# Optimization experiments

Measured on AMD Instinct MI355X. Metric: run time of the kernel, lower is better.

## Reference

```python
import jax, jax.numpy as jnp
import numpy as np

N_NODES = 8192
N_EDGES = 65536
MUL = 16          # multiplicity of 0e and 1o irreps
NB = 16           # num_radial_basis
HID = 16          # num_radial_dimension
MAX_RADIUS = 5.0
SQRT3 = float(np.sqrt(3.0))


def soft_unit_step(x):
    # e3nn.math.soft_unit_step: exp(-1/x) for x>0 else 0 (grad-safe where)
    safe = jnp.where(x > 0, x, 1.0)
    return jnp.where(x > 0, jnp.exp(-1.0 / safe), 0.0)


def setup_inputs() -> dict:
    key = jax.random.key(0)
    ks = jax.random.split(key, 12)
    f_in = jax.random.normal(ks[0], (N_NODES, 4 * MUL), jnp.float32)
    edge_vec = jax.random.normal(ks[1], (N_EDGES, 3), jnp.float32) * 1.5
    edge_src = jax.random.randint(ks[2], (N_EDGES,), 0, N_NODES)
    edge_dst = jax.random.randint(ks[3], (N_EDGES,), 0, N_NODES)
    Wq0 = jax.random.normal(ks[4], (MUL, MUL), jnp.float32)
    Wq1 = jax.random.normal(ks[5], (MUL, MUL), jnp.float32)
    Wk1 = jax.random.normal(ks[6], (NB, HID), jnp.float32)
    Wk2 = jax.random.normal(ks[7], (HID, 4 * MUL * MUL), jnp.float32)
    Wv1 = jax.random.normal(ks[8], (NB, HID), jnp.float32)
    Wv2 = jax.random.normal(ks[9], (HID, 4 * MUL * MUL), jnp.float32)
    Wd0 = jax.random.normal(ks[10], (MUL, MUL), jnp.float32)
    Wd1 = jax.random.normal(ks[11], (MUL, MUL), jnp.float32)
    return dict(f_in=f_in, edge_vec=edge_vec, edge_src=edge_src, edge_dst=edge_dst,
                Wq0=Wq0, Wq1=Wq1, Wk1=Wk1, Wk2=Wk2, Wv1=Wv1, Wv2=Wv2, Wd0=Wd0, Wd1=Wd1)


def _forward(f_in, edge_vec, edge_src, edge_dst,
             Wq0, Wq1, Wk1, Wk2, Wv1, Wv2, Wd0, Wd1):
    f0 = f_in[:, :MUL]                         # [N, MUL]    0e scalars
    f1 = f_in[:, MUL:].reshape(-1, MUL, 3)     # [N, MUL, 3] 1o vectors

    r = jnp.linalg.norm(edge_vec, axis=1)      # [E]
    u = edge_vec / r[:, None]
    sh1 = SQRT3 * u                            # Y_1, component norm (|Y1|^2 = 3); Y_0 = 1

    # soft_one_hot_linspace, basis='smooth_finite', cutoff=True, * sqrt(NB)
    values = jnp.linspace(0.0, MAX_RADIUS, NB + 2)
    step = values[1] - values[0]
    diff = (r[:, None] - values[1:-1]) / step
    C = 1.14136 * float(np.exp(2.0))
    rb = (C * soft_unit_step(diff + 1.0) * soft_unit_step(1.0 - diff)) * np.sqrt(NB)

    edge_cut = soft_unit_step(10.0 * (1.0 - r / MAX_RADIUS))  # [E]

    def mlp(x, W1, W2):  # e3nn FullyConnectedNet with fan-in normalization
        h = jax.nn.silu(x @ (W1 / np.sqrt(NB)))
        return h @ (W2 / np.sqrt(HID))

    wk = mlp(rb, Wk1, Wk2).reshape(-1, 4, MUL, MUL)  # per-edge TP weights
    wv = mlp(rb, Wv1, Wv2).reshape(-1, 4, MUL, MUL)

    # h_q: per-irrep linear
    q0 = f0 @ Wq0 / np.sqrt(MUL)
    q1 = jnp.einsum('nic,io->noc', f1, Wq1) / np.sqrt(MUL)

    x0 = f0[edge_src]   # [E, MUL]
    x1 = f1[edge_src]   # [E, MUL, 3]

    def fctp(w):
        # FullyConnectedTensorProduct (16x0e+16x1o) x (0e+1o) -> (16x0e+16x1o)
        # 4 paths: 0x0->0, 1x1->0 (dot/sqrt3), 0x1->1, 1x0->1
        a = 1.0 / np.sqrt(2 * MUL)
        o0 = jnp.einsum('eij,ei->ej', w[:, 0], x0) \
           + jnp.einsum('eij,eic,ec->ej', w[:, 1], x1, sh1) / SQRT3
        o1 = jnp.einsum('eij,ei,ec->ejc', w[:, 2], x0, sh1) \
           + jnp.einsum('eij,eic->ejc', w[:, 3], x1)
        return o0 * a, o1 * a

    k0, k1 = fctp(wk)
    v0, v1 = fctp(wv)

    # dot_product: FCTP(query, key) -> 0e
    ad = 1.0 / np.sqrt(2.0 * MUL * MUL)
    dot = ad * (jnp.einsum('ij,ei,ej->e', Wd0, q0[edge_dst], k0)
                + jnp.einsum('ij,eic,ejc->e', Wd1, q1[edge_dst], k1) / SQRT3)

    exp = edge_cut * jnp.exp(dot)                                   # [E]
    z = jax.ops.segment_sum(exp, edge_dst, num_segments=N_NODES)    # [N]
    z = jnp.where(z == 0.0, 1.0, z)
    alpha = exp / z[edge_dst]
    # alpha.relu().sqrt() with grad-safe sqrt at 0
    s = jnp.where(alpha > 0, jnp.sqrt(jnp.where(alpha > 0, alpha, 1.0)), 0.0)

    f_out0 = jax.ops.segment_sum(s[:, None] * v0, edge_dst, num_segments=N_NODES)
    f_out1 = jax.ops.segment_sum(s[:, None, None] * v1, edge_dst, num_segments=N_NODES)
    return jnp.concatenate([f_out0, f_out1.reshape(-1, MUL * 3)], axis=-1)  # [N, 64]


def reference(f_in, edge_vec, edge_src, edge_dst,
              Wq0, Wq1, Wk1, Wk2, Wv1, Wv2, Wd0, Wd1):
    return _forward(f_in, edge_vec, edge_src, edge_dst,
                    Wq0, Wq1, Wk1, Wk2, Wv1, Wv2, Wd0, Wd1)
```

## Files before the change

kernel.cpp:

```cpp
#include <hip/hip_runtime.h>
#include <hip/hip_bf16.h>

#define N_NODES 8192
#define N_EDGES 65536
#define BUCKET  48

#define CNT_OFF  0
#define WF_OFF   8192
#define QDI_OFF  24576
#define EXP_OFF  548864
#define VH_OFF   942080

typedef _Float16 half8 __attribute__((ext_vector_type(8)));
typedef float f32x4 __attribute__((ext_vector_type(4)));

__device__ __forceinline__ float sus_f(float x) { return x > 0.f ? __expf(-1.f / x) : 0.f; }
__device__ __forceinline__ float silu_f(float x) { return x / (1.f + __expf(-x)); }

__device__ __forceinline__ half8 vmul(half8 v, _Float16 s) {
    half8 r;
#pragma unroll
    for (int d = 0; d < 8; ++d) r[d] = v[d] * s;
    return r;
}

__global__ __launch_bounds__(256) void k_prep(
    const float* __restrict__ f_in,
    const float* __restrict__ Wq0, const float* __restrict__ Wq1,
    const float* __restrict__ Wd0, const float* __restrict__ Wd1,
    const float* __restrict__ Wk2, const float* __restrict__ Wv2,
    half8* __restrict__ wfrag, float* __restrict__ qdi) {
    __shared__ float f0s[16][16];
    __shared__ float f1s[16][48];
    __shared__ float t0s[16][16];
    __shared__ float t1s[16][48];
    const int blk = blockIdx.x;
    const int tid = threadIdx.x;

    if (blk < 16) {
        int g = blk * 256 + tid;
        int lane = g & 63, t = (g >> 6) & 7, b = (g >> 9) & 3, kv = g >> 11;
        const float* src = kv ? Wv2 : Wk2;
        int n = lane & 15, quad = lane >> 4;
        const float SC = 0.044194173824159216f;
        half8 out;
#pragma unroll
        for (int d = 0; d < 8; ++d) {
            int k = t * 32 + quad * 8 + d;
            int i = k & 15, h = k >> 4;
            out[d] = (_Float16)(src[h * 1024 + b * 256 + i * 16 + n] * SC);
        }
        wfrag[g] = out;
        return;
    }
    const int j = tid & 15, ln = tid >> 4;
    const int n = (blk - 16) * 16 + ln;
    f0s[ln][j]         = f_in[n * 64 + j];
    f1s[ln][j * 3 + 0] = f_in[n * 64 + 16 + j * 3 + 0];
    f1s[ln][j * 3 + 1] = f_in[n * 64 + 16 + j * 3 + 1];
    f1s[ln][j * 3 + 2] = f_in[n * 64 + 16 + j * 3 + 2];
    __syncthreads();
    float t0 = 0.f, ta = 0.f, tb = 0.f, tc = 0.f;
#pragma unroll
    for (int p = 0; p < 16; ++p) {
        float wq0 = Wq0[p * 16 + j];
        float wq1 = Wq1[p * 16 + j];
        t0 += f0s[ln][p] * wq0;
        ta += f1s[ln][p * 3 + 0] * wq1;
        tb += f1s[ln][p * 3 + 1] * wq1;
        tc += f1s[ln][p * 3 + 2] * wq1;
    }
    t0s[ln][j] = t0;
    t1s[ln][j * 3 + 0] = ta; t1s[ln][j * 3 + 1] = tb; t1s[ln][j * 3 + 2] = tc;
    __syncthreads();
    float q0a = 0.f, qa = 0.f, qb = 0.f, qc = 0.f;
#pragma unroll
    for (int i = 0; i < 16; ++i) {
        float wd0 = Wd0[i * 16 + j];
        float wd1 = Wd1[i * 16 + j];
        q0a += t0s[ln][i] * wd0;
        qa  += t1s[ln][i * 3 + 0] * wd1;
        qb  += t1s[ln][i * 3 + 1] * wd1;
        qc  += t1s[ln][i * 3 + 2] * wd1;
    }
    const float S0 = 0.011048543456f;
    const float S1 = 0.0063788674817f;
    float4 q = {q0a * S0, qa * S1, qb * S1, qc * S1};
    ((float4*)qdi)[n * 16 + j] = q;
}

__global__ __launch_bounds__(256) void k_edge(
    const float* __restrict__ f_in, const float* __restrict__ evec,
    const int* __restrict__ esrc, const int* __restrict__ edst,
    const float* __restrict__ Wk1, const float* __restrict__ Wv1,
    const half8* __restrict__ wfrag,
    const float* __restrict__ qdi,
    int* __restrict__ cursor, float* __restrict__ expbuf, _Float16* __restrict__ vh) {
    __shared__ __align__(16) char s_arena[19456];
    _Float16 (*s_x0h)[24] = (_Float16(*)[24])(s_arena);
    _Float16 (*s_xsh)[24] = (_Float16(*)[24])(s_arena + 3072);
    _Float16 (*s_x1h0)[24] = (_Float16(*)[24])(s_arena + 6144);
    _Float16 (*s_x1h1)[24] = (_Float16(*)[24])(s_arena + 9216);
    _Float16 (*s_x1h2)[24] = (_Float16(*)[24])(s_arena + 12288);
    _Float16 (*s_hkh)[16] = (_Float16(*)[16])(s_arena + 15360);
    _Float16 (*s_hvh)[16] = (_Float16(*)[16])(s_arena + 17408);
    _Float16 (*s_vt)[72]  = (_Float16(*)[72])(s_arena);
    __shared__ float s_rb[64][16];
    __shared__ float s_sh[64][4];
    __shared__ int   s_slot[64];

    const int tid = threadIdx.x;
    const int e0 = blockIdx.x * 64;

    {
        const int el = tid >> 2, q = tid & 3;
        const int e = e0 + el;
        float v0 = evec[e * 3 + 0];
        float v1 = evec[e * 3 + 1];
        float v2 = evec[e * 3 + 2];
        float r = sqrtf(v0 * v0 + v1 * v1 + v2 * v2);
        float rs = r * 3.4f;
#pragma unroll
        for (int bb = 0; bb < 4; ++bb) {
            int b = q * 4 + bb;
            s_rb[el][b] = 33.734292f * sus_f(rs - (float)b) * sus_f((float)(b + 2) - rs);
        }
        if (q == 0) {
            float inv = r > 0.f ? 1.f / r : 0.f;
            const float SQ3 = 1.7320508075688772f;
            s_sh[el][0] = SQ3 * v0 * inv;
            s_sh[el][1] = SQ3 * v1 * inv;
            s_sh[el][2] = SQ3 * v2 * inv;
            s_sh[el][3] = sus_f(10.f - 2.f * r);
        }
    }
    __syncthreads();

    {
        const int j = tid & 15, slot = tid >> 4;
        _Float16* xp = (_Float16*)(s_arena + 6144);
#pragma unroll
        for (int s = 0; s < 4; ++s) {
            const int el = slot * 4 + s;
            const int e = e0 + el;
            float aK = 0.f, aV = 0.f;
#pragma unroll
            for (int b = 0; b < 16; ++b) {
                float rbv = s_rb[el][b];
                aK += rbv * Wk1[b * 16 + j];
                aV += rbv * Wv1[b * 16 + j];
            }
            s_hkh[el][(j & 1) * 8 + (j >> 1)] = (_Float16)silu_f(aK * 0.25f);
            s_hvh[el][(j & 1) * 8 + (j >> 1)] = (_Float16)silu_f(aV * 0.25f);
            const int src = esrc[e];
            float4 v4 = ((const float4*)f_in)[src * 16 + j];
            if (j < 4) {
#pragma unroll
                for (int d = 0; d < 4; ++d)
                    s_x0h[el][j * 4 + d] = (_Float16)((&v4.x)[d]);
            } else {
                const int cc = j * 4 - 16;
#pragma unroll
                for (int d = 0; d < 4; ++d) {
                    int c = cc + d;
                    int i = c / 3, comp = c - 3 * i;
                    xp[comp * 1536 + el * 24 + i] = (_Float16)((&v4.x)[d]);
                }
            }
        }
    }
    __syncthreads();

    {
        const int j = tid & 15, slot = tid >> 4;
#pragma unroll
        for (int s = 0; s < 4; ++s) {
            const int el = slot * 4 + s;
            float xa = (float)s_x1h0[el][j];
            float xb = (float)s_x1h1[el][j];
            float xc = (float)s_x1h2[el][j];
            s_xsh[el][j] = (_Float16)((xa * s_sh[el][0] + xb * s_sh[el][1] + xc * s_sh[el][2])
                                      * 0.57735026919f);
        }
    }
    __syncthreads();

    const int lane = tid & 63;
    const int wv = tid >> 6;
    const int m = lane & 15, quad = lane >> 4;
    const int eb = wv * 16;
    const int eloc = eb + m;
    const int ihalf = quad >> 1;
    const int hh = (quad & 1) * 8;

    half8 X0 = *(const half8*)&s_x0h[eloc][hh];
    half8 XS = *(const half8*)&s_xsh[eloc][hh];
    half8 Xa = *(const half8*)&s_x1h0[eloc][hh];
    half8 Xb = *(const half8*)&s_x1h1[eloc][hh];
    half8 Xc = *(const half8*)&s_x1h2[eloc][hh];
    half8 HK = *(const half8*)&s_hkh[eloc][ihalf * 8];
    half8 HV = *(const half8*)&s_hvh[eloc][ihalf * 8];
    __syncthreads();

    {
        f32x4 o0 = {0.f, 0.f, 0.f, 0.f}, a1 = o0, ax = o0, ay = o0, az = o0;
#pragma unroll
        for (int t = 0; t < 8; ++t) {
            _Float16 hs = HK[t];
            half8 B0 = wfrag[(0 * 8 + t) * 64 + lane];
            half8 B1 = wfrag[(1 * 8 + t) * 64 + lane];
            half8 B2 = wfrag[(2 * 8 + t) * 64 + lane];
            half8 B3 = wfrag[(3 * 8 + t) * 64 + lane];
            half8 A0 = vmul(X0, hs);
            half8 As = vmul(XS, hs);
            half8 Aa = vmul(Xa, hs);
            half8 Ab = vmul(Xb, hs);
            half8 Ac = vmul(Xc, hs);
            o0 = __builtin_amdgcn_mfma_f32_16x16x32_f16(A0, B0, o0, 0, 0, 0);
            o0 = __builtin_amdgcn_mfma_f32_16x16x32_f16(As, B1, o0, 0, 0, 0);
            a1 = __builtin_amdgcn_mfma_f32_16x16x32_f16(A0, B2, a1, 0, 0, 0);
            ax = __builtin_amdgcn_mfma_f32_16x16x32_f16(Aa, B3, ax, 0, 0, 0);
            ay = __builtin_amdgcn_mfma_f32_16x16x32_f16(Ab, B3, ay, 0, 0, 0);
            az = __builtin_amdgcn_mfma_f32_16x16x32_f16(Ac, B3, az, 0, 0, 0);
        }
        const int j = m;
#pragma unroll
        for (int r = 0; r < 4; ++r) {
            const int el = eb + quad * 4 + r;
            const int e = e0 + el;
            const int dst = edst[e];
            float sh0 = s_sh[el][0], sh1 = s_sh[el][1], sh2 = s_sh[el][2];
            float k1x = a1[r] * sh0 + ax[r];
            float k1y = a1[r] * sh1 + ay[r];
            float k1z = a1[r] * sh2 + az[r];
            float4 q = ((const float4*)qdi)[dst * 16 + j];
            float dp = q.x * o0[r] + q.y * k1x + q.z * k1y + q.w * k1z;
            dp += __shfl_xor(dp, 1);
            dp += __shfl_xor(dp, 2);
            dp += __shfl_xor(dp, 4);
            dp += __shfl_xor(dp, 8);
            if (j == 0) {
                float ev = s_sh[el][3] * __expf(dp);
                int local = atomicAdd(cursor + dst, 1);
                int slot = dst * BUCKET + local;
                s_slot[el] = slot;
                expbuf[slot] = ev;
            }
        }
    }

    {
        f32x4 o0 = {0.f, 0.f, 0.f, 0.f}, a1 = o0, ax = o0, ay = o0, az = o0;
        const half8* wfv = wfrag + 32 * 64;
#pragma unroll
        for (int t = 0; t < 8; ++t) {
            _Float16 hs = HV[t];
            half8 B0 = wfv[(0 * 8 + t) * 64 + lane];
            half8 B1 = wfv[(1 * 8 + t) * 64 + lane];
            half8 B2 = wfv[(2 * 8 + t) * 64 + lane];
            half8 B3 = wfv[(3 * 8 + t) * 64 + lane];
            half8 A0 = vmul(X0, hs);
            half8 As = vmul(XS, hs);
            half8 Aa = vmul(Xa, hs);
            half8 Ab = vmul(Xb, hs);
            half8 Ac = vmul(Xc, hs);
            o0 = __builtin_amdgcn_mfma_f32_16x16x32_f16(A0, B0, o0, 0, 0, 0);
            o0 = __builtin_amdgcn_mfma_f32_16x16x32_f16(As, B1, o0, 0, 0, 0);
            a1 = __builtin_amdgcn_mfma_f32_16x16x32_f16(A0, B2, a1, 0, 0, 0);
            ax = __builtin_amdgcn_mfma_f32_16x16x32_f16(Aa, B3, ax, 0, 0, 0);
            ay = __builtin_amdgcn_mfma_f32_16x16x32_f16(Ab, B3, ay, 0, 0, 0);
            az = __builtin_amdgcn_mfma_f32_16x16x32_f16(Ac, B3, az, 0, 0, 0);
        }
        const int j = m;
#pragma unroll
        for (int r = 0; r < 4; ++r) {
            const int el = eb + quad * 4 + r;
            float sh0 = s_sh[el][0], sh1 = s_sh[el][1], sh2 = s_sh[el][2];
            s_vt[el][j] = (_Float16)o0[r];
            s_vt[el][16 + j * 3 + 0] = (_Float16)(a1[r] * sh0 + ax[r]);
            s_vt[el][16 + j * 3 + 1] = (_Float16)(a1[r] * sh1 + ay[r]);
            s_vt[el][16 + j * 3 + 2] = (_Float16)(a1[r] * sh2 + az[r]);
        }
    }
    __syncthreads();

#pragma unroll
    for (int pass = 0; pass < 2; ++pass) {
        int row = pass * 32 + (tid >> 3);
        int part = tid & 7;
        half8 val = *(const half8*)&s_vt[row][part * 8];
        int slot = s_slot[row];
        *(half8*)(vh + (size_t)slot * 64 + part * 8) = val;
    }
}

__global__ __launch_bounds__(256) void k_out(
    const int* __restrict__ cnt,
    const float* __restrict__ expbuf, const _Float16* __restrict__ vh,
    float* __restrict__ fout) {
    const int col = threadIdx.x & 63;
    const int n = blockIdx.x * 4 + (threadIdx.x >> 6);
    const int deg = cnt[n];
    const int s0 = n * BUCKET;
    float zs = 0.f;
    float acc = 0.f;
    for (int i = 0; i < deg; ++i) {
        float ev = expbuf[s0 + i];
        zs += ev;
        acc += sqrtf(ev) * (float)vh[(size_t)(s0 + i) * 64 + col];
    }
    float scale = zs > 0.f ? rsqrtf(zs) : 0.f;
    fout[n * 64 + col] = acc * scale;
}

extern "C" void kernel_launch(void* const* d_in, const int* in_sizes, int n_in,
                              void* d_out, int out_size, void* d_ws, size_t ws_size,
                              hipStream_t stream) {
    const float* f_in = (const float*)d_in[0];
    const float* evec = (const float*)d_in[1];
    const int* esrc = (const int*)d_in[2];
    const int* edst = (const int*)d_in[3];
    const float* Wq0 = (const float*)d_in[4];
    const float* Wq1 = (const float*)d_in[5];
    const float* Wk1 = (const float*)d_in[6];
    const float* Wk2 = (const float*)d_in[7];
    const float* Wv1 = (const float*)d_in[8];
    const float* Wv2 = (const float*)d_in[9];
    const float* Wd0 = (const float*)d_in[10];
    const float* Wd1 = (const float*)d_in[11];

    float* ws     = (float*)d_ws;
    int*   cnt    = (int*)(ws + CNT_OFF);
    half8* wfrag  = (half8*)(ws + WF_OFF);
    float* qdi    = ws + QDI_OFF;
    float* expb   = ws + EXP_OFF;
    _Float16* vh  = (_Float16*)(ws + VH_OFF);
    float* fout   = (float*)d_out;

    hipMemsetAsync(cnt, 0, (size_t)8192 * sizeof(int), stream);

    k_prep<<<528, 256, 0, stream>>>(f_in, Wq0, Wq1, Wd0, Wd1, Wk2, Wv2, wfrag, qdi);
    k_edge<<<N_EDGES / 64, 256, 0, stream>>>(f_in, evec, esrc, edst, Wk1, Wv1,
                                             wfrag, qdi, cnt, expb, vh);
    k_out<<<N_NODES / 4, 256, 0, stream>>>(cnt, expb, vh, fout);
}
```

Before: 110.5 us.

## Fold counter memset into prep kernel, compute XS in registers, prefetch queries

Removes the separate hipMemsetAsync by having one prep block zero the bucket counters, saving a launch. In the edge kernel the projected vector term XS is now built in registers from the per-edge spherical harmonics, which drops a shared-memory array, a pass and a barrier. Destination indices and query vectors are loaded before the MFMA loop so their global latency overlaps the matrix work. The risks are slightly lower precision from doing the projection in fp16 and higher register pressure from the prefetched queries.

```diff
diff --git a/kernel.cpp b/kernel.cpp
--- a/kernel.cpp
+++ b/kernel.cpp
@@ -29,7 +29,7 @@
     const float* __restrict__ Wq0, const float* __restrict__ Wq1,
     const float* __restrict__ Wd0, const float* __restrict__ Wd1,
     const float* __restrict__ Wk2, const float* __restrict__ Wv2,
-    half8* __restrict__ wfrag, float* __restrict__ qdi) {
+    half8* __restrict__ wfrag, float* __restrict__ qdi, int* __restrict__ cnt) {
     __shared__ float f0s[16][16];
     __shared__ float f1s[16][48];
     __shared__ float t0s[16][16];
@@ -53,6 +53,11 @@
         wfrag[g] = out;
         return;
     }
+    if (blk == 16) {
+        int4 z = {0, 0, 0, 0};
+#pragma unroll
+        for (int i = 0; i < 8; ++i) ((int4*)cnt)[tid * 8 + i] = z;
+    }
     const int j = tid & 15, ln = tid >> 4;
     const int n = (blk - 16) * 16 + ln;
     f0s[ln][j]         = f_in[n * 64 + j];
@@ -96,14 +101,13 @@
     const half8* __restrict__ wfrag,
     const float* __restrict__ qdi,
     int* __restrict__ cursor, float* __restrict__ expbuf, _Float16* __restrict__ vh) {
-    __shared__ __align__(16) char s_arena[19456];
+    __shared__ __align__(16) char s_arena[16384];
     _Float16 (*s_x0h)[24] = (_Float16(*)[24])(s_arena);
-    _Float16 (*s_xsh)[24] = (_Float16(*)[24])(s_arena + 3072);
-    _Float16 (*s_x1h0)[24] = (_Float16(*)[24])(s_arena + 6144);
-    _Float16 (*s_x1h1)[24] = (_Float16(*)[24])(s_arena + 9216);
-    _Float16 (*s_x1h2)[24] = (_Float16(*)[24])(s_arena + 12288);
-    _Float16 (*s_hkh)[16] = (_Float16(*)[16])(s_arena + 15360);
-    _Float16 (*s_hvh)[16] = (_Float16(*)[16])(s_arena + 17408);
+    _Float16 (*s_x1h0)[24] = (_Float16(*)[24])(s_arena + 3072);
+    _Float16 (*s_x1h1)[24] = (_Float16(*)[24])(s_arena + 6144);
+    _Float16 (*s_x1h2)[24] = (_Float16(*)[24])(s_arena + 9216);
+    _Float16 (*s_hkh)[16] = (_Float16(*)[16])(s_arena + 12288);
+    _Float16 (*s_hvh)[16] = (_Float16(*)[16])(s_arena + 14336);
     _Float16 (*s_vt)[72]  = (_Float16(*)[72])(s_arena);
     __shared__ float s_rb[64][16];
     __shared__ float s_sh[64][4];
@@ -138,7 +142,7 @@
 
     {
         const int j = tid & 15, slot = tid >> 4;
-        _Float16* xp = (_Float16*)(s_arena + 6144);
+        _Float16* xp = (_Float16*)(s_arena + 3072);
 #pragma unroll
         for (int s = 0; s < 4; ++s) {
             const int el = slot * 4 + s;
@@ -171,20 +175,6 @@
     }
     __syncthreads();
 
-    {
-        const int j = tid & 15, slot = tid >> 4;
-#pragma unroll
-        for (int s = 0; s < 4; ++s) {
-            const int el = slot * 4 + s;
-            float xa = (float)s_x1h0[el][j];
-            float xb = (float)s_x1h1[el][j];
-            float xc = (float)s_x1h2[el][j];
-            s_xsh[el][j] = (_Float16)((xa * s_sh[el][0] + xb * s_sh[el][1] + xc * s_sh[el][2])
-                                      * 0.57735026919f);
-        }
-    }
-    __syncthreads();
-
     const int lane = tid & 63;
     const int wv = tid >> 6;
     const int m = lane & 15, quad = lane >> 4;
@@ -194,15 +184,30 @@
     const int hh = (quad & 1) * 8;
 
     half8 X0 = *(const half8*)&s_x0h[eloc][hh];
-    half8 XS = *(const half8*)&s_xsh[eloc][hh];
     half8 Xa = *(const half8*)&s_x1h0[eloc][hh];
     half8 Xb = *(const half8*)&s_x1h1[eloc][hh];
     half8 Xc = *(const half8*)&s_x1h2[eloc][hh];
     half8 HK = *(const half8*)&s_hkh[eloc][ihalf * 8];
     half8 HV = *(const half8*)&s_hvh[eloc][ihalf * 8];
-    __syncthreads();
-
-    {
+    half8 XS;
+    {
+        _Float16 u0 = (_Float16)(s_sh[eloc][0] * 0.57735026919f);
+        _Float16 u1 = (_Float16)(s_sh[eloc][1] * 0.57735026919f);
+        _Float16 u2 = (_Float16)(s_sh[eloc][2] * 0.57735026919f);
+#pragma unroll
+        for (int d = 0; d < 8; ++d) XS[d] = Xa[d] * u0 + Xb[d] * u1 + Xc[d] * u2;
+    }
+    __syncthreads();
+
+    {
+        int dsts[4];
+        float4 qv[4];
+#pragma unroll
+        for (int r = 0; r < 4; ++r) {
+            const int e = e0 + eb + quad * 4 + r;
+            dsts[r] = edst[e];
+            qv[r] = ((const float4*)qdi)[dsts[r] * 16 + m];
+        }
         f32x4 o0 = {0.f, 0.f, 0.f, 0.f}, a1 = o0, ax = o0, ay = o0, az = o0;
 #pragma unroll
         for (int t = 0; t < 8; ++t) {
@@ -227,13 +232,11 @@
 #pragma unroll
         for (int r = 0; r < 4; ++r) {
             const int el = eb + quad * 4 + r;
-            const int e = e0 + el;
-            const int dst = edst[e];
             float sh0 = s_sh[el][0], sh1 = s_sh[el][1], sh2 = s_sh[el][2];
             float k1x = a1[r] * sh0 + ax[r];
             float k1y = a1[r] * sh1 + ay[r];
             float k1z = a1[r] * sh2 + az[r];
-            float4 q = ((const float4*)qdi)[dst * 16 + j];
+            float4 q = qv[r];
             float dp = q.x * o0[r] + q.y * k1x + q.z * k1y + q.w * k1z;
             dp += __shfl_xor(dp, 1);
             dp += __shfl_xor(dp, 2);
@@ -241,8 +244,8 @@
             dp += __shfl_xor(dp, 8);
             if (j == 0) {
                 float ev = s_sh[el][3] * __expf(dp);
-                int local = atomicAdd(cursor + dst, 1);
-                int slot = dst * BUCKET + local;
+                int local = atomicAdd(cursor + dsts[r], 1);
+                int slot = dsts[r] * BUCKET + local;
                 s_slot[el] = slot;
                 expbuf[slot] = ev;
             }
@@ -337,9 +340,7 @@
     _Float16* vh  = (_Float16*)(ws + VH_OFF);
     float* fout   = (float*)d_out;
 
-    hipMemsetAsync(cnt, 0, (size_t)8192 * sizeof(int), stream);
-
-    k_prep<<<528, 256, 0, stream>>>(f_in, Wq0, Wq1, Wd0, Wd1, Wk2, Wv2, wfrag, qdi);
+    k_prep<<<528, 256, 0, stream>>>(f_in, Wq0, Wq1, Wd0, Wd1, Wk2, Wv2, wfrag, qdi, cnt);
     k_edge<<<N_EDGES / 64, 256, 0, stream>>>(f_in, evec, esrc, edst, Wk1, Wv1,
                                              wfrag, qdi, cnt, expb, vh);
     k_out<<<N_NODES / 4, 256, 0, stream>>>(cnt, expb, vh, fout);
```

New measurement: 110.2 us (median of 2 runs). About the same (-0.3%).
